# Kernel optimization log

Measured on AMD Instinct MI355X. Metric: run time of the kernel, lower is better.

## Reference

```python
import jax, jax.numpy as jnp
import numpy as np

INF = 10000.0


def setup_inputs() -> dict:
    key = jax.random.key(0)
    ks = jax.random.split(key, 4)
    bs, seqlen, hidden = 8, 512, 768
    head_size, heads = 64, 12
    inputs = jax.random.normal(ks[0], (bs, seqlen, hidden), dtype=jnp.float32)
    attention_mask = jnp.ones((bs, seqlen), dtype=jnp.int32)
    W1 = jax.random.normal(ks[1], (hidden, head_size * 2), dtype=jnp.float32) * 0.02
    b1 = jnp.zeros((head_size * 2,), dtype=jnp.float32)
    W2 = jax.random.normal(ks[2], (head_size * 2, heads * 2), dtype=jnp.float32) * 0.02
    b2 = jnp.zeros((heads * 2,), dtype=jnp.float32)
    return {"inputs": inputs, "attention_mask": attention_mask,
            "W1": W1, "b1": b1, "W2": W2, "b2": b2}


def _rope(t, sin, cos):
    # t: [b, s, d]; sin/cos: [s, d//2]
    t1, t2 = t[..., 0::2], t[..., 1::2]
    return jnp.stack([t1 * cos - t2 * sin, t1 * sin + t2 * cos], axis=-1).reshape(t.shape)


def reference(inputs, attention_mask, W1, b1, W2, b2):
    bs, seqlen = inputs.shape[:2]
    head_size = W1.shape[1] // 2
    x = inputs @ W1 + b1                      # [b, s, 2*head_size]
    qw, kw = x[..., 0::2], x[..., 1::2]       # [b, s, head_size] each
    # rotary embedding (computed like the buffer in the torch module)
    pos = jnp.arange(seqlen, dtype=jnp.float32)
    inv_freq = 1.0 / (10000.0 ** (jnp.arange(0, head_size, 2, dtype=jnp.float32) / head_size))
    freqs = pos[:, None] * inv_freq[None, :]  # [s, head_size//2]
    sin, cos = jnp.sin(freqs), jnp.cos(freqs)
    qw = _rope(qw, sin, cos)
    kw = _rope(kw, sin, cos)
    logits = jnp.einsum('bmd,bnd->bmn', qw, kw) / (head_size ** 0.5)  # [b, s, s]
    bias = (x @ W2 + b2).transpose(0, 2, 1) / 2.0                      # [b, 2*heads, s]
    logits = logits[:, None] + bias[:, ::2, None, :] + bias[:, 1::2, :, None]  # [b, h, s, s]
    am = attention_mask.astype(logits.dtype)
    mask = 1.0 - am[:, None, None, :] * am[:, None, :, None]           # [b, 1, s, s]
    logits = logits - mask * INF
    # tril mask: positions with end < start (j < i)
    idx = jnp.arange(seqlen)
    tril = (idx[None, :] < idx[:, None]).astype(logits.dtype)[None, None]  # [1, 1, s, s]
    logits = logits - tril * INF
    mask_out = jnp.logical_or(mask.astype(bool),
                              jnp.broadcast_to(tril.astype(bool), (bs, 1, seqlen, seqlen)))
    return logits, mask_out
```

## Files before the change

### kernel.cpp

```cpp
#include <hip/hip_runtime.h>

#define BSZ 8
#define SEQ 512
#define HID 768
#define N1 128
#define N2 24
#define HS 64
#define HEADS 12
#define INFV 10000.0f

typedef __attribute__((ext_vector_type(8))) short s8b;
typedef __attribute__((ext_vector_type(4))) float f32x4;

__device__ __forceinline__ unsigned short f2bf(float f) {
    union { float f; unsigned int u; } c; c.f = f;
    unsigned int u = c.u;
    u += 0x7FFFu + ((u >> 16) & 1u);
    return (unsigned short)(u >> 16);
}

__device__ __forceinline__ s8b loadB(const float* __restrict__ wsrc) {
    union { s8b v; unsigned short u[8]; } r;
#pragma unroll
    for (int i = 0; i < 8; ++i) r.u[i] = f2bf(wsrc[i * N1]);
    return r.v;
}

#define ASLOT(chunk, r) (((chunk) * 16 + ((r) ^ ((chunk) & 7))) * 8)

__global__ __launch_bounds__(512, 4) void k1_proj(
    const float* __restrict__ inp, const float* __restrict__ W1,
    const float* __restrict__ b1, const float* __restrict__ W2,
    const float* __restrict__ b2,
    float* __restrict__ qw, float* __restrict__ kwT,
    float* __restrict__ bP0, float* __restrict__ bP1)
{
    __shared__ unsigned short aF[96 * 16 * 8];
    __shared__ float ps[16][64];
    __shared__ float xs[16][72];
    __shared__ float kT[32][17];

    const int tid = threadIdx.x;
    const int rt = blockIdx.x >> 1;
    const int ch = blockIdx.x & 1;
    const int row0 = rt * 16;
    const int b = row0 >> 9;
    const int m0 = row0 & 511;

    {
        const float4* src = (const float4*)(inp + (size_t)row0 * HID);
#pragma unroll
        for (int i = 0; i < 6; ++i) {
            int f4 = tid + i * 512;
            int r = f4 / 192;
            int c4 = f4 % 192;
            float4 v = src[f4];
            int chunk = c4 >> 1;
            int half = c4 & 1;
            ushort4 w;
            w.x = f2bf(v.x); w.y = f2bf(v.y); w.z = f2bf(v.z); w.w = f2bf(v.w);
            *(ushort4*)&aF[ASLOT(chunk, r) + half * 4] = w;
        }
    }
    __syncthreads();

    const int wv = tid >> 6;
    const int ln = tid & 63;
    const int lr = ln & 15;
    const int lg = ln >> 4;
    const int w3 = wv & 3;
    const int kh = wv >> 2;
    const int cg = ch * 64 + w3 * 16 + lr;

    const float* wbase = W1 + (size_t)(kh * 384 + lg * 8) * N1 + cg;

    f32x4 acc = {0.f, 0.f, 0.f, 0.f};
    s8b bA = loadB(wbase);
    s8b bB = loadB(wbase + 32 * N1);

#define AFRAG(kc) (*(const s8b*)&aF[ASLOT((kh * 12 + (kc)) * 4 + lg, lr)])
#pragma unroll
    for (int kc = 0; kc < 12; kc += 2) {
        acc = __builtin_amdgcn_mfma_f32_16x16x32_bf16(AFRAG(kc), bA, acc, 0, 0, 0);
        if (kc + 2 < 12) bA = loadB(wbase + (size_t)(kc + 2) * 32 * N1);
        acc = __builtin_amdgcn_mfma_f32_16x16x32_bf16(AFRAG(kc + 1), bB, acc, 0, 0, 0);
        if (kc + 3 < 12) bB = loadB(wbase + (size_t)(kc + 3) * 32 * N1);
    }
#undef AFRAG

    if (kh == 1) {
#pragma unroll
        for (int g = 0; g < 4; ++g) ps[lg * 4 + g][w3 * 16 + lr] = acc[g];
    }
    __syncthreads();
    if (kh == 0) {
        float b1v = b1[cg];
#pragma unroll
        for (int g = 0; g < 4; ++g)
            xs[lg * 4 + g][w3 * 16 + lr] = acc[g] + ps[lg * 4 + g][w3 * 16 + lr] + b1v;
    }
    __syncthreads();

    if (tid < 16 * N2) {
        int r = tid / N2, c = tid - r * N2;
        const float* w2p = W2 + (size_t)(ch * 64) * N2 + c;
        float dot = (ch == 0) ? b2[c] : 0.0f;
#pragma unroll 8
        for (int kl = 0; kl < 64; ++kl)
            dot = fmaf(xs[r][kl], w2p[kl * N2], dot);
        float* bP = ch ? bP1 : bP0;
        bP[(size_t)(b * N2 + c) * SEQ + m0 + r] = dot * 0.5f;
    }

    if (tid < 256) {
        const int r = tid >> 4, jj = tid & 15;
        const int j = ch * 16 + jj;
        const int m = m0 + r;
        const float C = 0.4152410118609203f;
        float invf = exp2f(-(float)j * C);
        float ang = (float)m * invf;
        float sv = __sinf(ang), cv = __cosf(ang);
        float4 xv = *(const float4*)&xs[r][4 * jj];
        float rq0 = xv.x * cv - xv.z * sv;
        float rq1 = xv.x * sv + xv.z * cv;
        float rk0 = xv.y * cv - xv.w * sv;
        float rk1 = xv.y * sv + xv.w * cv;
        *(float2*)(qw + (size_t)(b * SEQ + m) * HS + 2 * j) = make_float2(rq0, rq1);
        kT[2 * jj][r]     = rk0;
        kT[2 * jj + 1][r] = rk1;
    }
    __syncthreads();

    if (tid < 256) {
        int dl = tid >> 3, q = tid & 7;
        float2 v = *(const float2*)&kT[dl][2 * q];
        *(float2*)(kwT + (size_t)(b * HS + ch * 32 + dl) * SEQ + m0 + 2 * q) = v;
    }
}

__global__ __launch_bounds__(256) void k2_out(
    const float* __restrict__ qw, const float* __restrict__ kwT,
    const float* __restrict__ bP0, const float* __restrict__ bP1,
    const int* __restrict__ am, float* __restrict__ out)
{
    __shared__ float q_lds[8][HS];
    __shared__ float bo[8][HEADS];
    __shared__ int amm[8];

    const int tid = threadIdx.x;
    const int b = blockIdx.x >> 6;
    const int m0 = (blockIdx.x & 63) * 8;

#pragma unroll
    for (int i = 0; i < 2; ++i) {
        int idx = tid + i * 256;
        q_lds[idx >> 6][idx & 63] = qw[(size_t)(b * SEQ + m0) * HS + idx];
    }
    if (tid < 96) {
        int r = tid / 12, h = tid - r * 12;
        size_t ix = (size_t)(b * N2 + 2 * h + 1) * SEQ + m0 + r;
        bo[r][h] = bP0[ix] + bP1[ix];
    }
    if (tid < 8) amm[tid] = am[b * SEQ + m0 + tid];
    __syncthreads();

    const int n0 = tid * 2;
    float qk0[8] = {0, 0, 0, 0, 0, 0, 0, 0};
    float qk1[8] = {0, 0, 0, 0, 0, 0, 0, 0};

#pragma unroll
    for (int dc = 0; dc < 2; ++dc) {
        float2 kn[32];
#pragma unroll
        for (int d = 0; d < 32; ++d)
            kn[d] = *(const float2*)&kwT[(size_t)(b * HS + dc * 32 + d) * SEQ + n0];
#pragma unroll
        for (int r = 0; r < 8; ++r) {
#pragma unroll
            for (int d4 = 0; d4 < 8; ++d4) {
                float4 qv = *(const float4*)&q_lds[r][dc * 32 + d4 * 4];
                qk0[r] = fmaf(qv.x, kn[d4 * 4 + 0].x, qk0[r]);
                qk0[r] = fmaf(qv.y, kn[d4 * 4 + 1].x, qk0[r]);
                qk0[r] = fmaf(qv.z, kn[d4 * 4 + 2].x, qk0[r]);
                qk0[r] = fmaf(qv.w, kn[d4 * 4 + 3].x, qk0[r]);
                qk1[r] = fmaf(qv.x, kn[d4 * 4 + 0].y, qk1[r]);
                qk1[r] = fmaf(qv.y, kn[d4 * 4 + 1].y, qk1[r]);
                qk1[r] = fmaf(qv.z, kn[d4 * 4 + 2].y, qk1[r]);
                qk1[r] = fmaf(qv.w, kn[d4 * 4 + 3].y, qk1[r]);
            }
        }
    }

    const int amn0 = am[b * SEQ + n0];
    const int amn1 = am[b * SEQ + n0 + 1];
    float pen0[8], pen1[8];
    float2 mo[8];
#pragma unroll
    for (int r = 0; r < 8; ++r) {
        int m = m0 + r;
        float msk0 = (1.0f - (float)(amn0 * amm[r])) * INFV;
        float msk1 = (1.0f - (float)(amn1 * amm[r])) * INFV;
        pen0[r] = msk0 + ((n0 < m) ? INFV : 0.0f);
        pen1[r] = msk1 + ((n0 + 1 < m) ? INFV : 0.0f);
        bool b0 = (amn0 * amm[r] != 1) || (n0 < m);
        bool b1m = (amn1 * amm[r] != 1) || (n0 + 1 < m);
        mo[r].x = b0 ? 1.0f : 0.0f;
        mo[r].y = b1m ? 1.0f : 0.0f;
    }

    float2 be[HEADS];
#pragma unroll
    for (int h = 0; h < HEADS; ++h) {
        size_t ix = (size_t)(b * N2 + 2 * h) * SEQ + n0;
        float2 e0 = *(const float2*)&bP0[ix];
        float2 e1 = *(const float2*)&bP1[ix];
        be[h] = make_float2(e0.x + e1.x, e0.y + e1.y);
    }

    const size_t obase = (size_t)b * HEADS * SEQ * SEQ + n0;
#pragma unroll
    for (int h = 0; h < HEADS; ++h) {
#pragma unroll
        for (int r = 0; r < 8; ++r) {
            float2 v;
            v.x = fmaf(qk0[r], 0.125f, be[h].x + bo[r][h]) - pen0[r];
            v.y = fmaf(qk1[r], 0.125f, be[h].y + bo[r][h]) - pen1[r];
            *(float2*)&out[obase + ((size_t)h * SEQ + m0 + r) * SEQ] = v;
        }
    }
    const size_t mbase = (size_t)BSZ * HEADS * SEQ * SEQ
                       + ((size_t)b * SEQ + m0) * SEQ + n0;
#pragma unroll
    for (int r = 0; r < 8; ++r)
        *(float2*)&out[mbase + (size_t)r * SEQ] = mo[r];
}

extern "C" void kernel_launch(void* const* d_in, const int* in_sizes, int n_in,
                              void* d_out, int out_size, void* d_ws, size_t ws_size,
                              hipStream_t stream) {
    const float* inp = (const float*)d_in[0];
    const int*   am  = (const int*)d_in[1];
    const float* W1  = (const float*)d_in[2];
    const float* b1  = (const float*)d_in[3];
    const float* W2  = (const float*)d_in[4];
    const float* b2  = (const float*)d_in[5];

    float* ws    = (float*)d_ws;
    float* qw    = ws;
    float* kwT   = ws + 262144;
    float* bP0   = ws + 524288;
    float* bP1   = ws + 622592;

    float* out = (float*)d_out;

    hipLaunchKernelGGL(k1_proj, dim3(512), dim3(512), 0, stream,
                       inp, W1, b1, W2, b2, qw, kwT, bP0, bP1);
    hipLaunchKernelGGL(k2_out, dim3(4096 / 8), dim3(256), 0, stream,
                       qw, kwT, bP0, bP1, am, out);
}
```

Baseline: 40.10 us.

## Fuse projection and output kernels into one persistent kernel with a grid barrier

The two launches are merged into a single kernel of 256 blocks. Each block runs two projection jobs, then waits at a grid-wide barrier built on an atomic counter, then runs two output jobs. Shared memory for the two phases is overlaid in a union. The output phase now has each of 512 threads handle one column with scalar stores, instead of 256 threads handling column pairs with float2 stores. This aims to remove the kernel-launch gap between the phases. In exchange it adds a memset launch, a spin barrier that needs all blocks to be resident at once, and less work in flight during the projection phase.

```diff
diff --git a/kernel.cpp b/kernel.cpp
--- a/kernel.cpp
+++ b/kernel.cpp
@@ -8,9 +8,23 @@
 #define HS 64
 #define HEADS 12
 #define INFV 10000.0f
+#define NBLK 256
 
 typedef __attribute__((ext_vector_type(8))) short s8b;
 typedef __attribute__((ext_vector_type(4))) float f32x4;
+
+struct SharedA {
+    unsigned short aF[96 * 16 * 8];
+    float ps[16][64];
+    float xs[16][72];
+    float kT[32][17];
+};
+struct SharedB {
+    float q_lds[8][HS];
+    float bo[8][HEADS];
+    int amm[8];
+};
+union SharedU { SharedA a; SharedB b; };
 
 __device__ __forceinline__ unsigned short f2bf(float f) {
     union { float f; unsigned int u; } c; c.f = f;
@@ -28,21 +42,16 @@
 
 #define ASLOT(chunk, r) (((chunk) * 16 + ((r) ^ ((chunk) & 7))) * 8)
 
-__global__ __launch_bounds__(512, 4) void k1_proj(
+__device__ __forceinline__ void phaseA(
+    int job, int tid, SharedA& s,
     const float* __restrict__ inp, const float* __restrict__ W1,
     const float* __restrict__ b1, const float* __restrict__ W2,
     const float* __restrict__ b2,
     float* __restrict__ qw, float* __restrict__ kwT,
     float* __restrict__ bP0, float* __restrict__ bP1)
 {
-    __shared__ unsigned short aF[96 * 16 * 8];
-    __shared__ float ps[16][64];
-    __shared__ float xs[16][72];
-    __shared__ float kT[32][17];
-
-    const int tid = threadIdx.x;
-    const int rt = blockIdx.x >> 1;
-    const int ch = blockIdx.x & 1;
+    const int rt = job >> 1;
+    const int ch = job & 1;
     const int row0 = rt * 16;
     const int b = row0 >> 9;
     const int m0 = row0 & 511;
@@ -59,7 +68,7 @@
             int half = c4 & 1;
             ushort4 w;
             w.x = f2bf(v.x); w.y = f2bf(v.y); w.z = f2bf(v.z); w.w = f2bf(v.w);
-            *(ushort4*)&aF[ASLOT(chunk, r) + half * 4] = w;
+            *(ushort4*)&s.aF[ASLOT(chunk, r) + half * 4] = w;
         }
     }
     __syncthreads();
@@ -78,7 +87,7 @@
     s8b bA = loadB(wbase);
     s8b bB = loadB(wbase + 32 * N1);
 
-#define AFRAG(kc) (*(const s8b*)&aF[ASLOT((kh * 12 + (kc)) * 4 + lg, lr)])
+#define AFRAG(kc) (*(const s8b*)&s.aF[ASLOT((kh * 12 + (kc)) * 4 + lg, lr)])
 #pragma unroll
     for (int kc = 0; kc < 12; kc += 2) {
         acc = __builtin_amdgcn_mfma_f32_16x16x32_bf16(AFRAG(kc), bA, acc, 0, 0, 0);
@@ -90,14 +99,14 @@
 
     if (kh == 1) {
 #pragma unroll
-        for (int g = 0; g < 4; ++g) ps[lg * 4 + g][w3 * 16 + lr] = acc[g];
+        for (int g = 0; g < 4; ++g) s.ps[lg * 4 + g][w3 * 16 + lr] = acc[g];
     }
     __syncthreads();
     if (kh == 0) {
         float b1v = b1[cg];
 #pragma unroll
         for (int g = 0; g < 4; ++g)
-            xs[lg * 4 + g][w3 * 16 + lr] = acc[g] + ps[lg * 4 + g][w3 * 16 + lr] + b1v;
+            s.xs[lg * 4 + g][w3 * 16 + lr] = acc[g] + s.ps[lg * 4 + g][w3 * 16 + lr] + b1v;
     }
     __syncthreads();
 
@@ -107,7 +116,7 @@
         float dot = (ch == 0) ? b2[c] : 0.0f;
 #pragma unroll 8
         for (int kl = 0; kl < 64; ++kl)
-            dot = fmaf(xs[r][kl], w2p[kl * N2], dot);
+            dot = fmaf(s.xs[r][kl], w2p[kl * N2], dot);
         float* bP = ch ? bP1 : bP0;
         bP[(size_t)(b * N2 + c) * SEQ + m0 + r] = dot * 0.5f;
     }
@@ -120,119 +129,129 @@
         float invf = exp2f(-(float)j * C);
         float ang = (float)m * invf;
         float sv = __sinf(ang), cv = __cosf(ang);
-        float4 xv = *(const float4*)&xs[r][4 * jj];
+        float4 xv = *(const float4*)&s.xs[r][4 * jj];
         float rq0 = xv.x * cv - xv.z * sv;
         float rq1 = xv.x * sv + xv.z * cv;
         float rk0 = xv.y * cv - xv.w * sv;
         float rk1 = xv.y * sv + xv.w * cv;
         *(float2*)(qw + (size_t)(b * SEQ + m) * HS + 2 * j) = make_float2(rq0, rq1);
-        kT[2 * jj][r]     = rk0;
-        kT[2 * jj + 1][r] = rk1;
+        s.kT[2 * jj][r]     = rk0;
+        s.kT[2 * jj + 1][r] = rk1;
     }
     __syncthreads();
 
     if (tid < 256) {
         int dl = tid >> 3, q = tid & 7;
-        float2 v = *(const float2*)&kT[dl][2 * q];
+        float2 v = *(const float2*)&s.kT[dl][2 * q];
         *(float2*)(kwT + (size_t)(b * HS + ch * 32 + dl) * SEQ + m0 + 2 * q) = v;
     }
 }
 
-__global__ __launch_bounds__(256) void k2_out(
+__device__ __forceinline__ void phaseB(
+    int job, int tid, SharedB& s,
     const float* __restrict__ qw, const float* __restrict__ kwT,
     const float* __restrict__ bP0, const float* __restrict__ bP1,
     const int* __restrict__ am, float* __restrict__ out)
 {
-    __shared__ float q_lds[8][HS];
-    __shared__ float bo[8][HEADS];
-    __shared__ int amm[8];
-
-    const int tid = threadIdx.x;
-    const int b = blockIdx.x >> 6;
-    const int m0 = (blockIdx.x & 63) * 8;
-
-#pragma unroll
-    for (int i = 0; i < 2; ++i) {
-        int idx = tid + i * 256;
-        q_lds[idx >> 6][idx & 63] = qw[(size_t)(b * SEQ + m0) * HS + idx];
-    }
+    const int b = job >> 6;
+    const int m0 = (job & 63) * 8;
+
+    s.q_lds[tid >> 6][tid & 63] = qw[(size_t)(b * SEQ + m0) * HS + tid];
     if (tid < 96) {
         int r = tid / 12, h = tid - r * 12;
         size_t ix = (size_t)(b * N2 + 2 * h + 1) * SEQ + m0 + r;
-        bo[r][h] = bP0[ix] + bP1[ix];
-    }
-    if (tid < 8) amm[tid] = am[b * SEQ + m0 + tid];
-    __syncthreads();
-
-    const int n0 = tid * 2;
-    float qk0[8] = {0, 0, 0, 0, 0, 0, 0, 0};
-    float qk1[8] = {0, 0, 0, 0, 0, 0, 0, 0};
+        s.bo[r][h] = bP0[ix] + bP1[ix];
+    }
+    if (tid < 8) s.amm[tid] = am[b * SEQ + m0 + tid];
+    __syncthreads();
+
+    const int n = tid;
+    float qk[8] = {0, 0, 0, 0, 0, 0, 0, 0};
 
 #pragma unroll
     for (int dc = 0; dc < 2; ++dc) {
-        float2 kn[32];
+        float kn[32];
 #pragma unroll
         for (int d = 0; d < 32; ++d)
-            kn[d] = *(const float2*)&kwT[(size_t)(b * HS + dc * 32 + d) * SEQ + n0];
+            kn[d] = kwT[(size_t)(b * HS + dc * 32 + d) * SEQ + n];
 #pragma unroll
         for (int r = 0; r < 8; ++r) {
 #pragma unroll
             for (int d4 = 0; d4 < 8; ++d4) {
-                float4 qv = *(const float4*)&q_lds[r][dc * 32 + d4 * 4];
-                qk0[r] = fmaf(qv.x, kn[d4 * 4 + 0].x, qk0[r]);
-                qk0[r] = fmaf(qv.y, kn[d4 * 4 + 1].x, qk0[r]);
-                qk0[r] = fmaf(qv.z, kn[d4 * 4 + 2].x, qk0[r]);
-                qk0[r] = fmaf(qv.w, kn[d4 * 4 + 3].x, qk0[r]);
-                qk1[r] = fmaf(qv.x, kn[d4 * 4 + 0].y, qk1[r]);
-                qk1[r] = fmaf(qv.y, kn[d4 * 4 + 1].y, qk1[r]);
-                qk1[r] = fmaf(qv.z, kn[d4 * 4 + 2].y, qk1[r]);
-                qk1[r] = fmaf(qv.w, kn[d4 * 4 + 3].y, qk1[r]);
+                float4 qv = *(const float4*)&s.q_lds[r][dc * 32 + d4 * 4];
+                qk[r] = fmaf(qv.x, kn[d4 * 4 + 0], qk[r]);
+                qk[r] = fmaf(qv.y, kn[d4 * 4 + 1], qk[r]);
+                qk[r] = fmaf(qv.z, kn[d4 * 4 + 2], qk[r]);
+                qk[r] = fmaf(qv.w, kn[d4 * 4 + 3], qk[r]);
             }
         }
     }
 
-    const int amn0 = am[b * SEQ + n0];
-    const int amn1 = am[b * SEQ + n0 + 1];
-    float pen0[8], pen1[8];
-    float2 mo[8];
+    const int amn = am[b * SEQ + n];
+    float pen[8], mo[8];
 #pragma unroll
     for (int r = 0; r < 8; ++r) {
         int m = m0 + r;
-        float msk0 = (1.0f - (float)(amn0 * amm[r])) * INFV;
-        float msk1 = (1.0f - (float)(amn1 * amm[r])) * INFV;
-        pen0[r] = msk0 + ((n0 < m) ? INFV : 0.0f);
-        pen1[r] = msk1 + ((n0 + 1 < m) ? INFV : 0.0f);
-        bool b0 = (amn0 * amm[r] != 1) || (n0 < m);
-        bool b1m = (amn1 * amm[r] != 1) || (n0 + 1 < m);
-        mo[r].x = b0 ? 1.0f : 0.0f;
-        mo[r].y = b1m ? 1.0f : 0.0f;
-    }
-
-    float2 be[HEADS];
+        float msk = (1.0f - (float)(amn * s.amm[r])) * INFV;
+        pen[r] = msk + ((n < m) ? INFV : 0.0f);
+        mo[r] = ((amn * s.amm[r] != 1) || (n < m)) ? 1.0f : 0.0f;
+    }
+
+    float be[HEADS];
 #pragma unroll
     for (int h = 0; h < HEADS; ++h) {
-        size_t ix = (size_t)(b * N2 + 2 * h) * SEQ + n0;
-        float2 e0 = *(const float2*)&bP0[ix];
-        float2 e1 = *(const float2*)&bP1[ix];
-        be[h] = make_float2(e0.x + e1.x, e0.y + e1.y);
-    }
-
-    const size_t obase = (size_t)b * HEADS * SEQ * SEQ + n0;
+        size_t ix = (size_t)(b * N2 + 2 * h) * SEQ + n;
+        be[h] = bP0[ix] + bP1[ix];
+    }
+
+    const size_t obase = (size_t)b * HEADS * SEQ * SEQ + n;
 #pragma unroll
     for (int h = 0; h < HEADS; ++h) {
 #pragma unroll
         for (int r = 0; r < 8; ++r) {
-            float2 v;
-            v.x = fmaf(qk0[r], 0.125f, be[h].x + bo[r][h]) - pen0[r];
-            v.y = fmaf(qk1[r], 0.125f, be[h].y + bo[r][h]) - pen1[r];
-            *(float2*)&out[obase + ((size_t)h * SEQ + m0 + r) * SEQ] = v;
+            out[obase + ((size_t)h * SEQ + m0 + r) * SEQ] =
+                fmaf(qk[r], 0.125f, be[h] + s.bo[r][h]) - pen[r];
         }
     }
     const size_t mbase = (size_t)BSZ * HEADS * SEQ * SEQ
-                       + ((size_t)b * SEQ + m0) * SEQ + n0;
+                       + ((size_t)b * SEQ + m0) * SEQ + n;
 #pragma unroll
     for (int r = 0; r < 8; ++r)
-        *(float2*)&out[mbase + (size_t)r * SEQ] = mo[r];
+        out[mbase + (size_t)r * SEQ] = mo[r];
+}
+
+__global__ __launch_bounds__(512, 2) void fused_egp(
+    const float* __restrict__ inp, const float* __restrict__ W1,
+    const float* __restrict__ b1, const float* __restrict__ W2,
+    const float* __restrict__ b2, const int* __restrict__ am,
+    float* __restrict__ qw, float* __restrict__ kwT,
+    float* __restrict__ bP0, float* __restrict__ bP1,
+    unsigned int* __restrict__ ctr, float* __restrict__ out)
+{
+    __shared__ SharedU u;
+    const int tid = threadIdx.x;
+    const int bid = blockIdx.x;
+
+#pragma unroll
+    for (int j = 0; j < 2; ++j) {
+        if (j) __syncthreads();
+        phaseA(bid * 2 + j, tid, u.a, inp, W1, b1, W2, b2, qw, kwT, bP0, bP1);
+    }
+
+    __syncthreads();
+    __threadfence();
+    if (tid == 0)
+        __hip_atomic_fetch_add(ctr, 1u, __ATOMIC_RELEASE, __HIP_MEMORY_SCOPE_AGENT);
+    while (__hip_atomic_load(ctr, __ATOMIC_ACQUIRE, __HIP_MEMORY_SCOPE_AGENT) < NBLK)
+        __builtin_amdgcn_s_sleep(8);
+    __threadfence();
+    __syncthreads();
+
+#pragma unroll
+    for (int j = 0; j < 2; ++j) {
+        if (j) __syncthreads();
+        phaseB(bid * 2 + j, tid, u.b, qw, kwT, bP0, bP1, am, out);
+    }
 }
 
 extern "C" void kernel_launch(void* const* d_in, const int* in_sizes, int n_in,
@@ -250,11 +269,11 @@
     float* kwT   = ws + 262144;
     float* bP0   = ws + 524288;
     float* bP1   = ws + 622592;
+    unsigned int* ctr = (unsigned int*)(ws + 720896);
 
     float* out = (float*)d_out;
 
-    hipLaunchKernelGGL(k1_proj, dim3(512), dim3(512), 0, stream,
-                       inp, W1, b1, W2, b2, qw, kwT, bP0, bP1);
-    hipLaunchKernelGGL(k2_out, dim3(4096 / 8), dim3(256), 0, stream,
-                       qw, kwT, bP0, bP1, am, out);
-}
+    hipMemsetAsync(ctr, 0, sizeof(unsigned int), stream);
+    hipLaunchKernelGGL(fused_egp, dim3(NBLK), dim3(512), 0, stream,
+                       inp, W1, b1, W2, b2, am, qw, kwT, bP0, bP1, ctr, out);
+}
```

Result: slower. 156.7 us (+290.7%).
